# Kernel optimization log

Hardware: AMD Instinct MI355X
Metric: run time of the kernel (lower is better)

## Reference

```python
import jax, jax.numpy as jnp
import numpy as np

EPS = 1e-12  # F.normalize default eps


def setup_inputs() -> dict:
    key = jax.random.key(0)
    k1, k2 = jax.random.split(key)
    b, c, angRes, h, w = 4, 64, 5, 64, 64
    d = 64  # dims
    x = jax.random.normal(k1, (b, c, angRes * angRes, h, w), dtype=jnp.float32)
    # 1x1 conv weight [3*dims, channels] (kernel size 1, no bias)
    W = jax.random.normal(k2, (3 * d, c), dtype=jnp.float32) * 0.02
    return {"x": x, "W": W}


def reference(x, W):
    b, c, n, h, w = x.shape
    d = W.shape[0] // 3
    # 1x1 conv over angular (u,v) grid == channel matmul; rearranges are free reindexings
    qkv = jnp.einsum('oc,bcnhw->bonhw', W, x)  # [b, 3d, n, h, w]
    q, k, v = jnp.split(qkv, 3, axis=1)        # each [b, d, n, h, w]

    def flat(t):  # '(b h w) c u v -> b (u v) (c h w)'
        return t.transpose(0, 2, 1, 3, 4).reshape(b, n, d * h * w)

    q, k, v = flat(q), flat(k), flat(v)
    # L2-normalize along the (c h w) feature dim (k was normalized on dim=-2 of its
    # transposed layout, which is this same feature dim)
    q = q / jnp.maximum(jnp.linalg.norm(q, axis=-1, keepdims=True), EPS)
    k = k / jnp.maximum(jnp.linalg.norm(k, axis=-1, keepdims=True), EPS)
    att = jax.nn.softmax(jnp.einsum('bnf,bmf->bnm', q, k), axis=-1)  # [b, n, n], n=25
    out = jnp.einsum('bnm,bmf->bnf', att, v)   # [b, n, d*h*w]
    # 'b (u v) (c h w) -> b c (u v) h w'
    return out.reshape(b, n, d, h, w).transpose(0, 2, 1, 3, 4)
```

## Files before the change

kernel.cpp:

```cpp
#include <hip/hip_runtime.h>

#define B   4
#define C   64
#define D   64
#define NN  25
#define HW  4096
#define F   (D*HW)

#define PT  64
#define QCH 256
#define NCH 4

typedef unsigned short ushort_t;
typedef unsigned int   uint_t;
typedef __attribute__((ext_vector_type(8)))  short  short8;
typedef __attribute__((ext_vector_type(8)))  unsigned short us8;
typedef __attribute__((ext_vector_type(16))) float  floatx16;
typedef __attribute__((ext_vector_type(4)))  float  f32x4;
typedef __attribute__((ext_vector_type(4)))  unsigned short us4;

__device__ ushort_t g_Wthi[128 * C];
__device__ ushort_t g_Wtlo[128 * C];
__device__ ushort_t g_Wvhi[D * C];
__device__ ushort_t g_Wvlo[D * C];

__device__ float g_S[B * NN * NN];
__device__ float g_qq[B * NN];
__device__ float g_kk[B * NN];
__device__ float g_attT[B * NN * NN];

static __device__ __forceinline__ ushort_t f2bf(float f) {
    uint_t u = __float_as_uint(f);
    u += 0x7FFFu + ((u >> 16) & 1u);
    return (ushort_t)(u >> 16);
}
static __device__ __forceinline__ float bf2f(ushort_t h) {
    return __uint_as_float((uint_t)h << 16);
}

static __device__ __forceinline__ int lds_x(int p, int c) {
    return p * 64 + ((((c >> 3) ^ (p & 7)) << 3) | (c & 7));
}

__global__ void k_prep(const float* __restrict__ W) {
    int i = blockIdx.x * 256 + threadIdx.x;
    if (i < 2500)      g_S[i] = 0.f;
    else if (i < 2600) g_qq[i - 2500] = 0.f;
    else if (i < 2700) g_kk[i - 2600] = 0.f;
    if (i < 128 * 64) {
        float w = W[i];
        ushort_t hi = f2bf(w);
        g_Wthi[i] = hi;
        g_Wtlo[i] = f2bf(w - bf2f(hi));
    } else if (i < 192 * 64) {
        float w = W[i];
        int j = i - 128 * 64;
        ushort_t hi = f2bf(w);
        g_Wvhi[j] = hi;
        g_Wvlo[j] = f2bf(w - bf2f(hi));
    }
}

__global__ void __launch_bounds__(256, 4)
k_proj(const float* __restrict__ x,
       ushort_t* __restrict__ Q, ushort_t* __restrict__ K,
       float* __restrict__ V) {
    __shared__ ushort_t sXhi[PT * 64];
    __shared__ ushort_t sXlo[PT * 64];

    const int t  = threadIdx.x;
    const int wv = t >> 6, ln = t & 63;
    const int n  = blockIdx.y, b = blockIdx.z;
    const int tile = blockIdx.x;
    const int gp0  = tile * PT;
    const size_t cstride = (size_t)NN * HW;

    const int row = ln & 31, kh8 = (ln >> 5) * 8, d0 = wv * 32;
    short8 ahi[4], alo[4];
#pragma unroll
    for (int ks = 0; ks < 4; ++ks) {
        ahi[ks] = *(const short8*)&g_Wthi[(d0 + row) * 64 + ks * 16 + kh8];
        alo[ks] = *(const short8*)&g_Wtlo[(d0 + row) * 64 + ks * 16 + kh8];
    }

    {
        const int c16 = wv * 16;
#pragma unroll
        for (int cg = 0; cg < 4; ++cg) {
            const int c4 = c16 + cg * 4;
            const float* xc = x + ((size_t)(b * C + c4) * NN + n) * HW + gp0;
            float v[4];
#pragma unroll
            for (int i = 0; i < 4; ++i) v[i] = xc[(size_t)i * cstride + ln];
            us4 h, l;
#pragma unroll
            for (int i = 0; i < 4; ++i) {
                ushort_t hi = f2bf(v[i]);
                h[i] = hi;
                l[i] = f2bf(v[i] - bf2f(hi));
            }
            *(us4*)&sXhi[lds_x(ln, c4)] = h;
            *(us4*)&sXlo[lds_x(ln, c4)] = l;
        }
    }
    __syncthreads();

    ushort_t* __restrict__ O = (wv < 2) ? Q : K;
    const int slab = wv & 1;
    const size_t nbase = (size_t)(b * NN + n) * F;

    float nrm = 0.f;
#pragma unroll
    for (int pt = 0; pt < 2; ++pt) {
        const int pcol = pt * 32 + row;
        floatx16 acc;
#pragma unroll
        for (int r = 0; r < 16; ++r) acc[r] = 0.f;
#pragma unroll
        for (int ks = 0; ks < 4; ++ks) {
            const int c0 = ks * 16 + kh8;
            short8 bhi = *(const short8*)&sXhi[lds_x(pcol, c0)];
            short8 blo = *(const short8*)&sXlo[lds_x(pcol, c0)];
            acc = __builtin_amdgcn_mfma_f32_32x32x16_bf16(ahi[ks], bhi, acc, 0, 0, 0);
            acc = __builtin_amdgcn_mfma_f32_32x32x16_bf16(alo[ks], bhi, acc, 0, 0, 0);
            acc = __builtin_amdgcn_mfma_f32_32x32x16_bf16(ahi[ks], blo, acc, 0, 0, 0);
        }
#pragma unroll
        for (int r4 = 0; r4 < 4; ++r4) {
            us4 h;
#pragma unroll
            for (int j = 0; j < 4; ++j) {
                const float a = acc[r4 * 4 + j];
                nrm += a * a;
                h[j] = f2bf(a);
            }
            *(us4*)&O[nbase + (((size_t)((tile * 2 + slab) * 8 + pt * 4 + r4)) << 8)
                      + ln * 4] = h;
        }
    }
    for (int off = 32; off > 0; off >>= 1) nrm += __shfl_xor(nrm, off);
    if (ln == 0) atomicAdd(((wv < 2) ? g_qq : g_kk) + b * NN + n, nrm);

    {
        const int sv = wv & 1, ptv = (wv >> 1) & 1;
        short8 vhi[4], vlo[4];
#pragma unroll
        for (int ks = 0; ks < 4; ++ks) {
            vhi[ks] = *(const short8*)&g_Wvhi[(sv * 32 + row) * 64 + ks * 16 + kh8];
            vlo[ks] = *(const short8*)&g_Wvlo[(sv * 32 + row) * 64 + ks * 16 + kh8];
        }
        const int pcol = ptv * 32 + row;
        floatx16 av;
#pragma unroll
        for (int r = 0; r < 16; ++r) av[r] = 0.f;
#pragma unroll
        for (int ks = 0; ks < 4; ++ks) {
            const int c0 = ks * 16 + kh8;
            short8 bhi = *(const short8*)&sXhi[lds_x(pcol, c0)];
            short8 blo = *(const short8*)&sXlo[lds_x(pcol, c0)];
            av = __builtin_amdgcn_mfma_f32_32x32x16_bf16(vhi[ks], bhi, av, 0, 0, 0);
            av = __builtin_amdgcn_mfma_f32_32x32x16_bf16(vlo[ks], bhi, av, 0, 0, 0);
            av = __builtin_amdgcn_mfma_f32_32x32x16_bf16(vhi[ks], blo, av, 0, 0, 0);
        }
#pragma unroll
        for (int r4 = 0; r4 < 4; ++r4) {
            f32x4 vv;
#pragma unroll
            for (int j = 0; j < 4; ++j) vv[j] = av[r4 * 4 + j];
            *(f32x4*)&V[nbase + (((size_t)((tile * 4 + sv * 2 + ptv) * 4 + r4)) << 8)
                        + ln * 4] = vv;
        }
    }
}

__global__ void __launch_bounds__(512, 8)
k_sqk(const ushort_t* __restrict__ Q, const ushort_t* __restrict__ K) {
    __shared__ __align__(16) unsigned char smem[35904];
    ushort_t* sQ = (ushort_t*)smem;
    ushort_t* sK = (ushort_t*)(smem + 16384);
    float (*redS)[64][17] = (float (*)[64][17])smem;

    const int t  = threadIdx.x;
    const int wv = t >> 6, ln = t & 63;
    const int b  = blockIdx.y;
    const size_t fbase = (size_t)blockIdx.x * (QCH * NCH);

    const int col = t & 31;
    const int r0  = t >> 5;
    const int rr  = ln & 31;
    const int khalf = ln >> 5;

    floatx16 acc;
#pragma unroll
    for (int r = 0; r < 16; ++r) acc[r] = 0.f;

    for (int ch = 0; ch < NCH; ++ch) {
        const size_t f0 = fbase + (size_t)ch * QCH;
        if (ch) __syncthreads();
#pragma unroll
        for (int pass = 0; pass < 2; ++pass) {
            const int r  = pass * 16 + r0;
            const int rc = (r < NN) ? r : (NN - 1);
            const size_t g = ((size_t)b * NN + rc) * F + f0 + col * 8;
            const int lx = r * QCH + ((col ^ (r & 7)) * 8);
            *(us8*)&sQ[lx] = *(const us8*)(Q + g);
            *(us8*)&sK[lx] = *(const us8*)(K + g);
        }
        __syncthreads();
#pragma unroll
        for (int i = 0; i < 2; ++i) {
            const int cunit = (wv * 2 + i) * 2 + khalf;
            const int lx = rr * QCH + ((cunit ^ (rr & 7)) * 8);
            short8 aq = *(const short8*)&sQ[lx];
            short8 bk = *(const short8*)&sK[lx];
            acc = __builtin_amdgcn_mfma_f32_32x32x16_bf16(aq, bk, acc, 0, 0, 0);
        }
    }

    __syncthreads();
#pragma unroll
    for (int r = 0; r < 16; ++r) redS[wv][ln][r] = acc[r];
    __syncthreads();
    if (wv == 0) {
#pragma unroll
        for (int r = 0; r < 16; ++r) {
            float v = 0.f;
#pragma unroll
            for (int w = 0; w < 8; ++w) v += redS[w][ln][r];
            const int srow = (r & 3) + 8 * (r >> 2) + 4 * (ln >> 5);
            const int scol = ln & 31;
            if (srow < NN && scol < NN)
                atomicAdd(&g_S[((size_t)b * NN + srow) * NN + scol], v);
        }
    }
}

__global__ void k_softmax() {
    const int b = blockIdx.x, n = threadIdx.x;
    if (n >= NN) return;
    const float qn = fmaxf(sqrtf(g_qq[b * NN + n]), 1e-12f);
    float l[NN], mx = -1e30f;
#pragma unroll
    for (int m = 0; m < NN; ++m) {
        const float km = fmaxf(sqrtf(g_kk[b * NN + m]), 1e-12f);
        l[m] = g_S[((size_t)b * NN + n) * NN + m] / (qn * km);
        mx = fmaxf(mx, l[m]);
    }
    float s = 0.f;
#pragma unroll
    for (int m = 0; m < NN; ++m) { l[m] = expf(l[m] - mx); s += l[m]; }
    const float inv = 1.f / s;
#pragma unroll
    for (int m = 0; m < NN; ++m) g_attT[((size_t)b * NN + m) * NN + n] = l[m] * inv;
}

__global__ void __launch_bounds__(256, 4)
k_outmix(const float* __restrict__ V, float* __restrict__ out) {
    const int tid = blockIdx.x * 256 + threadIdx.x;
    const int b   = blockIdx.y;
    const float* Vb = V + (size_t)b * NN * F + (size_t)tid * 4;
    const float* at = g_attT + b * NN * NN;

    f32x4 acc[NN];
#pragma unroll
    for (int n = 0; n < NN; ++n) acc[n] = 0.f;
#pragma unroll 5
    for (int m = 0; m < NN; ++m) {
        const f32x4 v = *(const f32x4*)(Vb + (size_t)m * F);
#pragma unroll
        for (int n = 0; n < NN; ++n) acc[n] += at[m * NN + n] * v;
    }

    const int ln = tid & 63, c0 = tid >> 6;
    const int r4 = c0 & 3, ptv = (c0 >> 2) & 1, sv = (c0 >> 3) & 1;
    const int tile = c0 >> 4;
    const int p  = tile * 64 + ptv * 32 + (ln & 31);
    const int db = sv * 32 + 8 * r4 + 4 * (ln >> 5);
#pragma unroll
    for (int n = 0; n < NN; ++n)
#pragma unroll
        for (int j = 0; j < 4; ++j)
            out[((size_t)(b * D + db + j) * NN + n) * HW + p] = acc[n][j];
}

extern "C" void kernel_launch(void* const* d_in, const int* in_sizes, int n_in,
                              void* d_out, int out_size, void* d_ws, size_t ws_size,
                              hipStream_t stream) {
    const float* x = (const float*)d_in[0];
    const float* W = (const float*)d_in[1];
    float* outf = (float*)d_out;

    ushort_t* Q = (ushort_t*)d_out;
    ushort_t* K = Q + (size_t)B * NN * F;
    float*    V = (float*)d_ws;

    k_prep   <<<dim3(48),               256, 0, stream>>>(W);
    k_proj   <<<dim3(HW/PT, NN, B),     256, 0, stream>>>(x, Q, K, V);
    k_sqk    <<<dim3(F/(QCH*NCH), B),   512, 0, stream>>>(Q, K);
    k_softmax<<<dim3(B),                 64, 0, stream>>>();
    k_outmix <<<dim3(F/1024, B),        256, 0, stream>>>(V, outf);
}
```

Measured before the change: 356.4 us.

## Double projection pixel tile to 128 and batch x loads before LDS conversion

Raises the k_proj pixel tile from 64 to 128. Each block now loads all of its x values into registers before converting to split bf16 and writing them to LDS, and the hoisted weight fragments are reused across twice as many MFMA tiles. The V storage layout and the index math in k_outmix are changed to match the new tile ordering. This halves the grid, amortizing per-block weight loads and atomics, at the cost of more registers and LDS per block and possibly lower occupancy.

```diff
diff --git a/kernel.cpp b/kernel.cpp
--- a/kernel.cpp
+++ b/kernel.cpp
@@ -7,7 +7,7 @@
 #define HW  4096
 #define F   (D*HW)
 
-#define PT  64
+#define PT  128
 #define QCH 256
 #define NCH 4
 
@@ -73,9 +73,45 @@
     const int n  = blockIdx.y, b = blockIdx.z;
     const int tile = blockIdx.x;
     const int gp0  = tile * PT;
+    const int row = ln & 31, kh8 = (ln >> 5) * 8;
     const size_t cstride = (size_t)NN * HW;
 
-    const int row = ln & 31, kh8 = (ln >> 5) * 8, d0 = wv * 32;
+    {
+        float v[32];
+        const int c16 = wv * 16;
+#pragma unroll
+        for (int cg = 0; cg < 4; ++cg) {
+            const int c4 = c16 + cg * 4;
+            const float* xc = x + ((size_t)(b * C + c4) * NN + n) * HW + gp0;
+#pragma unroll
+            for (int ph = 0; ph < 2; ++ph)
+#pragma unroll
+                for (int i = 0; i < 4; ++i)
+                    v[cg * 8 + ph * 4 + i] =
+                        xc[(size_t)i * cstride + ph * 64 + ln];
+        }
+#pragma unroll
+        for (int cg = 0; cg < 4; ++cg) {
+            const int c4 = c16 + cg * 4;
+#pragma unroll
+            for (int ph = 0; ph < 2; ++ph) {
+                const int p = ph * 64 + ln;
+                us4 h, l;
+#pragma unroll
+                for (int i = 0; i < 4; ++i) {
+                    const float val = v[cg * 8 + ph * 4 + i];
+                    const ushort_t hi = f2bf(val);
+                    h[i] = hi;
+                    l[i] = f2bf(val - bf2f(hi));
+                }
+                *(us4*)&sXhi[lds_x(p, c4)] = h;
+                *(us4*)&sXlo[lds_x(p, c4)] = l;
+            }
+        }
+    }
+    __syncthreads();
+
+    const int d0 = wv * 32;
     short8 ahi[4], alo[4];
 #pragma unroll
     for (int ks = 0; ks < 4; ++ks) {
@@ -83,35 +119,13 @@
         alo[ks] = *(const short8*)&g_Wtlo[(d0 + row) * 64 + ks * 16 + kh8];
     }
 
-    {
-        const int c16 = wv * 16;
-#pragma unroll
-        for (int cg = 0; cg < 4; ++cg) {
-            const int c4 = c16 + cg * 4;
-            const float* xc = x + ((size_t)(b * C + c4) * NN + n) * HW + gp0;
-            float v[4];
-#pragma unroll
-            for (int i = 0; i < 4; ++i) v[i] = xc[(size_t)i * cstride + ln];
-            us4 h, l;
-#pragma unroll
-            for (int i = 0; i < 4; ++i) {
-                ushort_t hi = f2bf(v[i]);
-                h[i] = hi;
-                l[i] = f2bf(v[i] - bf2f(hi));
-            }
-            *(us4*)&sXhi[lds_x(ln, c4)] = h;
-            *(us4*)&sXlo[lds_x(ln, c4)] = l;
-        }
-    }
-    __syncthreads();
-
     ushort_t* __restrict__ O = (wv < 2) ? Q : K;
-    const int slab = wv & 1;
+    const int slab = (wv < 2) ? wv : wv - 2;
     const size_t nbase = (size_t)(b * NN + n) * F;
 
     float nrm = 0.f;
 #pragma unroll
-    for (int pt = 0; pt < 2; ++pt) {
+    for (int pt = 0; pt < 4; ++pt) {
         const int pcol = pt * 32 + row;
         floatx16 acc;
 #pragma unroll
@@ -134,7 +148,7 @@
                 nrm += a * a;
                 h[j] = f2bf(a);
             }
-            *(us4*)&O[nbase + (((size_t)((tile * 2 + slab) * 8 + pt * 4 + r4)) << 8)
+            *(us4*)&O[nbase + (((size_t)((tile * 2 + slab) * 16 + pt * 4 + r4)) << 8)
                       + ln * 4] = h;
         }
     }
@@ -142,33 +156,36 @@
     if (ln == 0) atomicAdd(((wv < 2) ? g_qq : g_kk) + b * NN + n, nrm);
 
     {
-        const int sv = wv & 1, ptv = (wv >> 1) & 1;
+        const int sv = wv & 1, ph = wv >> 1;
         short8 vhi[4], vlo[4];
 #pragma unroll
         for (int ks = 0; ks < 4; ++ks) {
             vhi[ks] = *(const short8*)&g_Wvhi[(sv * 32 + row) * 64 + ks * 16 + kh8];
             vlo[ks] = *(const short8*)&g_Wvlo[(sv * 32 + row) * 64 + ks * 16 + kh8];
         }
-        const int pcol = ptv * 32 + row;
-        floatx16 av;
-#pragma unroll
-        for (int r = 0; r < 16; ++r) av[r] = 0.f;
-#pragma unroll
-        for (int ks = 0; ks < 4; ++ks) {
-            const int c0 = ks * 16 + kh8;
-            short8 bhi = *(const short8*)&sXhi[lds_x(pcol, c0)];
-            short8 blo = *(const short8*)&sXlo[lds_x(pcol, c0)];
-            av = __builtin_amdgcn_mfma_f32_32x32x16_bf16(vhi[ks], bhi, av, 0, 0, 0);
-            av = __builtin_amdgcn_mfma_f32_32x32x16_bf16(vlo[ks], bhi, av, 0, 0, 0);
-            av = __builtin_amdgcn_mfma_f32_32x32x16_bf16(vhi[ks], blo, av, 0, 0, 0);
-        }
-#pragma unroll
-        for (int r4 = 0; r4 < 4; ++r4) {
-            f32x4 vv;
-#pragma unroll
-            for (int j = 0; j < 4; ++j) vv[j] = av[r4 * 4 + j];
-            *(f32x4*)&V[nbase + (((size_t)((tile * 4 + sv * 2 + ptv) * 4 + r4)) << 8)
-                        + ln * 4] = vv;
+#pragma unroll
+        for (int pt = 0; pt < 2; ++pt) {
+            const int pcol = ph * 64 + pt * 32 + row;
+            floatx16 av;
+#pragma unroll
+            for (int r = 0; r < 16; ++r) av[r] = 0.f;
+#pragma unroll
+            for (int ks = 0; ks < 4; ++ks) {
+                const int c0 = ks * 16 + kh8;
+                short8 bhi = *(const short8*)&sXhi[lds_x(pcol, c0)];
+                short8 blo = *(const short8*)&sXlo[lds_x(pcol, c0)];
+                av = __builtin_amdgcn_mfma_f32_32x32x16_bf16(vhi[ks], bhi, av, 0, 0, 0);
+                av = __builtin_amdgcn_mfma_f32_32x32x16_bf16(vlo[ks], bhi, av, 0, 0, 0);
+                av = __builtin_amdgcn_mfma_f32_32x32x16_bf16(vhi[ks], blo, av, 0, 0, 0);
+            }
+#pragma unroll
+            for (int r4 = 0; r4 < 4; ++r4) {
+                f32x4 vv;
+#pragma unroll
+                for (int j = 0; j < 4; ++j) vv[j] = av[r4 * 4 + j];
+                *(f32x4*)&V[nbase + (((size_t)((((tile * 2 + sv) * 2 + ph) * 2 + pt) * 4
+                    + r4)) << 8) + ln * 4] = vv;
+            }
         }
     }
 }
@@ -272,9 +289,9 @@
     }
 
     const int ln = tid & 63, c0 = tid >> 6;
-    const int r4 = c0 & 3, ptv = (c0 >> 2) & 1, sv = (c0 >> 3) & 1;
-    const int tile = c0 >> 4;
-    const int p  = tile * 64 + ptv * 32 + (ln & 31);
+    const int r4 = c0 & 3, ptv = (c0 >> 2) & 1, ph = (c0 >> 3) & 1;
+    const int sv = (c0 >> 4) & 1, tile = c0 >> 5;
+    const int p  = tile * 128 + ph * 64 + ptv * 32 + (ln & 31);
     const int db = sv * 32 + 8 * r4 + 4 * (ln >> 5);
 #pragma unroll
     for (int n = 0; n < NN; ++n)
```

New measurement: 301.6 us. 15.4% less time.
